# Optimization experiments

Hardware: AMD Instinct MI355X
Metric: run time of the kernel (lower is better)

The kernel has to match this reference:

```python
import jax, jax.numpy as jnp
import numpy as np

NUM_HEADS = 16
HEAD_DIM = 64
D_MODEL = NUM_HEADS * HEAD_DIM


def setup_inputs() -> dict:
    key = jax.random.key(0)
    ks = jax.random.split(key, 7)
    B, S = 2, 2048
    q = jax.random.normal(ks[0], (B, S, D_MODEL), dtype=jnp.float32)
    k = jax.random.normal(ks[1], (B, S, D_MODEL), dtype=jnp.float32)
    v = jax.random.normal(ks[2], (B, S, D_MODEL), dtype=jnp.float32)
    scale = 1.0 / np.sqrt(D_MODEL).astype(np.float32)
    w_q = jax.random.normal(ks[3], (D_MODEL, D_MODEL), dtype=jnp.float32) * scale
    w_k = jax.random.normal(ks[4], (D_MODEL, D_MODEL), dtype=jnp.float32) * scale
    w_v = jax.random.normal(ks[5], (D_MODEL, D_MODEL), dtype=jnp.float32) * scale
    w_o = jax.random.normal(ks[6], (D_MODEL, D_MODEL), dtype=jnp.float32) * scale
    return {"q": q, "k": k, "v": v, "w_q": w_q, "w_k": w_k, "w_v": w_v, "w_o": w_o}


def reference(q, k, v, w_q, w_k, w_v, w_o):
    B, S, _ = q.shape
    H, D = NUM_HEADS, HEAD_DIM
    # projections; q scaled by 1/sqrt(dim) as in the original (dim = per-head dim)
    qh = (q @ w_q) / jnp.sqrt(jnp.asarray(D, q.dtype))
    kh = k @ w_k
    vh = v @ w_v
    # tf.split(axis=-1) into H chunks == reshape [B,S,H,D]
    qh = qh.reshape(B, S, H, D)
    kh = kh.reshape(B, S, H, D)
    vh = vh.reshape(B, S, H, D)
    # keras Attention: scores = q @ k^T, softmax over keys, @ v (no extra scale)
    scores = jnp.einsum("bqhd,bkhd->bhqk", qh, kh)
    probs = jax.nn.softmax(scores, axis=-1)
    o = jnp.einsum("bhqk,bkhd->bqhd", probs, vh)
    o = o.reshape(B, S, H * D)
    return o @ w_o
```

## Files before the change

### kernel.cpp

```cpp
#include <hip/hip_runtime.h>
#include <hip/hip_bf16.h>


using bf16x8 = __attribute__((ext_vector_type(8))) short;
using f32x4  = __attribute__((ext_vector_type(4))) float;
using u32x4  = __attribute__((ext_vector_type(4))) unsigned;
typedef unsigned short u16;
using u16x4 = __attribute__((ext_vector_type(4))) u16;
using u16x8 = __attribute__((ext_vector_type(8))) u16;

#define GLDS16(g, l) __builtin_amdgcn_global_load_lds( \
    (const __attribute__((address_space(1))) void*)(g), \
    (__attribute__((address_space(3))) void*)(l), 16, 0, 0)

#if __has_builtin(__builtin_amdgcn_exp2f)
#define EXP2(x) __builtin_amdgcn_exp2f(x)
#else
#define EXP2(x) exp2f(x)
#endif

__device__ __forceinline__ void block_sync() {
  __builtin_amdgcn_sched_barrier(0);
  asm volatile("" ::: "memory");
  __builtin_amdgcn_s_barrier();
  asm volatile("" ::: "memory");
  __builtin_amdgcn_sched_barrier(0);
}

__device__ __forceinline__ u16 f2bf(float f) {
  unsigned u = __builtin_bit_cast(unsigned, f);
  u += 0x7fffu + ((u >> 16) & 1u);
  return (u16)(u >> 16);
}

__device__ __forceinline__ unsigned cvt_pk_bf16(float lo, float hi) {
  unsigned r;
  asm("v_cvt_pk_bf16_f32 %0, %1, %2" : "=v"(r) : "v"(lo), "v"(hi));
  return r;
}

__device__ __forceinline__ float fmax3(float a, float b, float c) {
  return fmaxf(fmaxf(a, b), c);
}

__global__ __launch_bounds__(256) void wtrans_kernel(
    const float* __restrict__ wq, const float* __restrict__ wk,
    const float* __restrict__ wv, const float* __restrict__ wo,
    u16* __restrict__ dst) {
  __shared__ float t[32][33];
  const int z = blockIdx.z;
  const float* src = (z == 0) ? wq : (z == 1) ? wk : (z == 2) ? wv : wo;
  u16* d = dst + (size_t)z * 1024 * 1024;
  const int tx = threadIdx.x & 31, ty = threadIdx.x >> 5;
  const int bx = blockIdx.x * 32, by = blockIdx.y * 32;
#pragma unroll
  for (int j = 0; j < 4; j++)
    t[ty + j * 8][tx] = src[(size_t)(by + ty + j * 8) * 1024 + bx + tx];
  __syncthreads();
#pragma unroll
  for (int j = 0; j < 4; j++)
    d[(size_t)(bx + ty + j * 8) * 1024 + by + tx] = f2bf(t[tx][ty + j * 8]);
}

__global__ __launch_bounds__(256, 3) void proj_kernel(
    const float* __restrict__ qf, const float* __restrict__ kf,
    const float* __restrict__ vf, const u16* __restrict__ WT,
    u16* __restrict__ Qh, u16* __restrict__ Kh, u16* __restrict__ Vt) {
  __shared__ u16 lds[24576];
  const int id = blockIdx.x;
  const int xcd = id & 7, l = id >> 3;
  const int z = l >> 5, rem = l & 31;
  const int by = xcd * 4 + (rem >> 3);
  const int bx = rem & 7;
  const int arow0 = by * 128, bcol0 = bx * 128;
  const float* A = (z == 0) ? qf : (z == 1) ? kf : vf;
  const u16* Bw = WT + (size_t)z * 1024 * 1024;

  const int tid = threadIdx.x;
  const int lane = tid & 63, wave = tid >> 6;
  const int lr = lane & 15, lg = lane >> 4;
  const int wr = (wave >> 1) * 64, wc = (wave & 1) * 64;
  const int ar = tid >> 3, ac = tid & 7;
  f32x4 acc[4][4] = {};

  f32x4 fa[4][2];
  u32x4 w[4];

  auto LOADA = [&](int kt) {
#pragma unroll
    for (int i = 0; i < 4; i++) {
      const float* ap = A + (size_t)(arow0 + i * 32 + ar) * 1024 + kt + ac * 8;
      fa[i][0] = *(const f32x4*)ap;
      fa[i][1] = *(const f32x4*)(ap + 4);
    }
  };
  auto GLDSB = [&](int kt, int nb) {
    u16* bd = lds + 8192 + nb * 8192;
#pragma unroll
    for (int i = 0; i < 4; i++) {
      int o = (i * 256 + tid) * 8;
      int row = o >> 6, ch = (o >> 3) & 7;
      int sc = (ch ^ (row & 7)) << 3;
      GLDS16(Bw + (size_t)(bcol0 + row) * 1024 + kt + sc, bd + o);
    }
  };
  auto CVT = [&]() {
#pragma unroll
    for (int i = 0; i < 4; i++) {
      u32x4 v = {cvt_pk_bf16(fa[i][0][0], fa[i][0][1]),
                 cvt_pk_bf16(fa[i][0][2], fa[i][0][3]),
                 cvt_pk_bf16(fa[i][1][0], fa[i][1][1]),
                 cvt_pk_bf16(fa[i][1][2], fa[i][1][3])};
      w[i] = v;
    }
  };
  auto WRITEA = [&]() {
#pragma unroll
    for (int i = 0; i < 4; i++) {
      int row = i * 32 + ar;
      *(u32x4*)&lds[row * 64 + ((ac ^ (row & 7)) << 3)] = w[i];
    }
  };
  auto MFMAK = [&](int cb) {
    const u16* Bb = lds + 8192 + cb * 8192;
#pragma unroll
    for (int kk = 0; kk < 2; kk++) {
      bf16x8 af[4], bfr[4];
      const int ke = kk * 32 + lg * 8;
#pragma unroll
      for (int m = 0; m < 4; m++) {
        int row = wr + m * 16 + lr;
        af[m] = *(const bf16x8*)&lds[row * 64 + (ke ^ ((row & 7) << 3))];
      }
#pragma unroll
      for (int n = 0; n < 4; n++) {
        int row = wc + n * 16 + lr;
        bfr[n] = *(const bf16x8*)&Bb[row * 64 + (ke ^ ((row & 7) << 3))];
      }
#pragma unroll
      for (int m = 0; m < 4; m++)
#pragma unroll
        for (int n = 0; n < 4; n++)
          acc[m][n] = __builtin_amdgcn_mfma_f32_16x16x32_bf16(af[m], bfr[n],
                                                              acc[m][n], 0, 0, 0);
    }
  };

#define PSTEP(KT, CB, MORE)                                                  \
  do {                                                                       \
    CVT();                                                                   \
    if (MORE) { LOADA((KT) + 64); GLDSB((KT) + 64, (CB) ^ 1); }              \
    WRITEA();                                                                \
    if (MORE)                                                                \
      asm volatile("s_waitcnt vmcnt(12) lgkmcnt(0)" ::: "memory");           \
    else                                                                     \
      asm volatile("s_waitcnt vmcnt(0) lgkmcnt(0)" ::: "memory");            \
    block_sync();                                                            \
    MFMAK(CB);                                                               \
    block_sync();                                                            \
  } while (0)

  LOADA(0);
  GLDSB(0, 0);
  for (int kt = 0; kt < 896; kt += 128) {
    PSTEP(kt, 0, true);
    PSTEP(kt + 64, 1, true);
  }
  PSTEP(896, 0, true);
  PSTEP(960, 1, false);
#undef PSTEP

  if (z == 2) {
    u16* T = lds;
    __syncthreads();
#pragma unroll
    for (int m = 0; m < 4; m++)
#pragma unroll
      for (int n = 0; n < 4; n++)
#pragma unroll
        for (int r = 0; r < 4; r++) {
          int sl = wr + m * 16 + lg * 4 + r;
          int cl = wc + n * 16 + lr;
          T[cl * 128 + (sl ^ ((cl & 7) << 3))] = f2bf(acc[m][n][r]);
        }
    __syncthreads();
    const int t = threadIdx.x;
    const int cl = t >> 1, s0 = (t & 1) * 64;
    const int gc = bcol0 + cl;
    const size_t vrow = ((size_t)(arow0 >> 11) * 16 + (gc >> 6)) * 64 + (gc & 63);
#pragma unroll
    for (int j = 0; j < 8; j++) {
      int sl = s0 + j * 8;
      u16x8 vv = *(const u16x8*)&T[cl * 128 + (sl ^ ((cl & 7) << 3))];
      *(u16x8*)&Vt[vrow * 2048 + (size_t)((arow0 & 2047) + sl)] = vv;
    }
  } else {
    const float scale = (z == 0) ? 0.18033688f : 1.0f;
    u16* dst = (z == 0) ? Qh : Kh;
#pragma unroll
    for (int m = 0; m < 4; m++)
#pragma unroll
      for (int n = 0; n < 4; n++)
#pragma unroll
        for (int r = 0; r < 4; r++) {
          int gr = arow0 + wr + m * 16 + lg * 4 + r;
          int gc = bcol0 + wc + n * 16 + lr;
          size_t idx = (((size_t)(gr >> 11) * 16 + (gc >> 6)) * 2048 +
                        (gr & 2047)) * 64 + (gc & 63);
          dst[idx] = f2bf(acc[m][n][r] * scale);
        }
  }
}

__global__ __launch_bounds__(512, 4) void attn_kernel(
    const u16* __restrict__ Qh, const u16* __restrict__ Kh,
    const u16* __restrict__ Vt, u16* __restrict__ Ob) {
  __shared__ u16 kt[4][64 * 64];
  __shared__ u16 vt[4][64 * 64];
  const int tid = threadIdx.x;
  const int lane = tid & 63, wave = tid >> 6;
  const int lr = lane & 15, lg = lane >> 4;
  const int id = blockIdx.x;
  const int swz = (id & 7) * 64 + (id >> 3);
  const int bh = swz >> 4;
  const int q0 = (swz & 15) * 128;
  const u16* Qb = Qh + ((size_t)bh * 2048 + q0) * 64;
  const u16* Kb = Kh + (size_t)bh * 2048 * 64;
  const u16* Vb = Vt + (size_t)bh * 64 * 2048;

  bf16x8 aq[2];
#pragma unroll
  for (int kk = 0; kk < 2; kk++)
    aq[kk] = *(const bf16x8*)(Qb + (wave * 16 + lr) * 64 + kk * 32 + lg * 8);

  const int hsw = (lr & 3) | (((lr >> 2) & 1) << 2);
  int koff[2][4];
#pragma unroll
  for (int n = 0; n < 4; n++) {
    int kr = 32 * (n >> 1) + 8 * (lr >> 2) + 4 * (n & 1) + (lr & 3);
#pragma unroll
    for (int kk = 0; kk < 2; kk++)
      koff[kk][n] = kr * 64 + ((kk * 32 + lg * 8) ^ (hsw << 3));
  }
  int voff[2][4];
#pragma unroll
  for (int n = 0; n < 4; n++) {
    int d = n * 16 + lr;
#pragma unroll
    for (int ks = 0; ks < 2; ks++)
      voff[ks][n] = d * 64 + ((ks * 32 + lg * 8) ^ ((d & 7) << 3));
  }

  const int o0 = tid * 8;
  const int srow = tid >> 3, sch = tid & 7;
  const int hk = (srow & 3) | (((srow >> 3) & 1) << 2);
  const u16* kg = Kb + (size_t)srow * 64 + ((sch ^ hk) << 3);
  const u16* vg = Vb + (size_t)srow * 2048 + ((sch ^ (srow & 7)) << 3);

  f32x4 oacc[4] = {};
  float mrun = -1e30f, lrun = 0.f;

  auto STAGE = [&](int t, int b) {
    GLDS16(kg + (size_t)t * 4096, &kt[0][0] + b * 4096 + o0);
    GLDS16(vg + t * 64, &vt[0][0] + b * 4096 + o0);
  };

  auto COMPUTE = [&](int cur) {
    f32x4 sacc[4] = {};
    __builtin_amdgcn_s_setprio(1);
#pragma unroll
    for (int kk = 0; kk < 2; kk++) {
#pragma unroll
      for (int n = 0; n < 4; n++) {
        bf16x8 ka = *(const bf16x8*)&kt[cur][koff[kk][n]];
        sacc[n] = __builtin_amdgcn_mfma_f32_16x16x32_bf16(ka, aq[kk],
                                                          sacc[n], 0, 0, 0);
      }
    }
    __builtin_amdgcn_s_setprio(0);
    float t0 = fmax3(sacc[0][0], sacc[0][1], sacc[0][2]);
    float t1 = fmax3(sacc[0][3], sacc[1][0], sacc[1][1]);
    float t2 = fmax3(sacc[1][2], sacc[1][3], sacc[2][0]);
    float t3 = fmax3(sacc[2][1], sacc[2][2], sacc[2][3]);
    float t4 = fmax3(sacc[3][0], sacc[3][1], sacc[3][2]);
    float mx = fmaxf(fmax3(t0, t1, t2), fmax3(t3, t4, sacc[3][3]));
    mx = fmaxf(mx, __shfl_xor(mx, 16));
    mx = fmaxf(mx, __shfl_xor(mx, 32));
    float mnew = fmaxf(mrun, mx);
    if (__all(mx - mrun <= 8.0f)) {
      mnew = mrun;
    } else {
      float corr = EXP2(mrun - mnew);
      mrun = mnew;
      lrun *= corr;
      float cr[4];
#pragma unroll
      for (int r = 0; r < 4; r++) cr[r] = __shfl(corr, lg * 4 + r);
#pragma unroll
      for (int n = 0; n < 4; n++)
#pragma unroll
        for (int r = 0; r < 4; r++) oacc[n][r] *= cr[r];
    }
    float psum = 0.f;
#pragma unroll
    for (int n = 0; n < 4; n++)
#pragma unroll
      for (int r = 0; r < 4; r++) {
        float p = EXP2(sacc[n][r] - mnew);
        sacc[n][r] = p;
        psum += p;
      }
    psum += __shfl_xor(psum, 16);
    psum += __shfl_xor(psum, 32);
    lrun += psum;
    u32x4 w0 = {cvt_pk_bf16(sacc[0][0], sacc[0][1]),
                cvt_pk_bf16(sacc[0][2], sacc[0][3]),
                cvt_pk_bf16(sacc[1][0], sacc[1][1]),
                cvt_pk_bf16(sacc[1][2], sacc[1][3])};
    u32x4 w1 = {cvt_pk_bf16(sacc[2][0], sacc[2][1]),
                cvt_pk_bf16(sacc[2][2], sacc[2][3]),
                cvt_pk_bf16(sacc[3][0], sacc[3][1]),
                cvt_pk_bf16(sacc[3][2], sacc[3][3])};
    bf16x8 pa0 = __builtin_bit_cast(bf16x8, w0);
    bf16x8 pa1 = __builtin_bit_cast(bf16x8, w1);
    __builtin_amdgcn_s_setprio(1);
#pragma unroll
    for (int ks = 0; ks < 2; ks++) {
      bf16x8 ap = ks ? pa1 : pa0;
      bf16x8 bv[4];
#pragma unroll
      for (int n = 0; n < 4; n++)
        bv[n] = *(const bf16x8*)&vt[cur][voff[ks][n]];
#pragma unroll
      for (int n = 0; n < 4; n++)
        oacc[n] = __builtin_amdgcn_mfma_f32_16x16x32_bf16(ap, bv[n],
                                                          oacc[n], 0, 0, 0);
    }
    __builtin_amdgcn_s_setprio(0);
  };

#define VMC6 asm volatile("s_waitcnt vmcnt(6)" ::: "memory")
#define VMC4 asm volatile("s_waitcnt vmcnt(4)" ::: "memory")
#define VMC2 asm volatile("s_waitcnt vmcnt(2)" ::: "memory")
#define VMC0 asm volatile("s_waitcnt vmcnt(0)" ::: "memory")
  STAGE(0, 0); STAGE(1, 1); STAGE(2, 2);
  for (int t = 0; t < 28; t += 4) {
    STAGE(t + 3, 3); VMC6; block_sync(); COMPUTE(0); block_sync();
    STAGE(t + 4, 0); VMC6; block_sync(); COMPUTE(1); block_sync();
    STAGE(t + 5, 1); VMC6; block_sync(); COMPUTE(2); block_sync();
    STAGE(t + 6, 2); VMC6; block_sync(); COMPUTE(3); block_sync();
  }
  STAGE(31, 3); VMC6; block_sync(); COMPUTE(0); block_sync();
  VMC4; block_sync(); COMPUTE(1); block_sync();
  VMC2; block_sync(); COMPUTE(2); block_sync();
  VMC0; block_sync(); COMPUTE(3);
#undef VMC6
#undef VMC4
#undef VMC2
#undef VMC0

  const int b = bh >> 4, h = bh & 15;
  float inv = 1.0f / lrun;
  float ivr[4];
#pragma unroll
  for (int r = 0; r < 4; r++) ivr[r] = __shfl(inv, lg * 4 + r);
#pragma unroll
  for (int r = 0; r < 4; r++) {
    int qrow = q0 + wave * 16 + lg * 4 + r;
#pragma unroll
    for (int n = 0; n < 4; n++) {
      int d = n * 16 + lr;
      Ob[((size_t)b * 2048 + qrow) * 1024 + h * 64 + d] = f2bf(oacc[n][r] * ivr[r]);
    }
  }
}

__global__ __launch_bounds__(256) void outproj_kernel(
    const u16* __restrict__ Ob, const u16* __restrict__ WoT,
    float* __restrict__ out) {
  __shared__ u16 ldsA[128 * 64];
  __shared__ u16 ldsB[64 * 64];
  const int tid = threadIdx.x;
  const int lane = tid & 63, wave = tid >> 6;
  const int lr = lane & 15, lg = lane >> 4;
  const int wr = (wave >> 1) * 64;
  const int wc = (wave & 1) * 32;
  const int id = blockIdx.x;
  const int xcd = id & 7, l = id >> 3;
  const int by = xcd * 4 + (l >> 4);
  const int bx = l & 15;
  const int arow0 = by * 128, bcol0 = bx * 64;
  f32x4 acc[4][2] = {};
  for (int kt = 0; kt < 1024; kt += 64) {
#pragma unroll
    for (int i = 0; i < 4; i++) {
      int o = (i * 256 + tid) * 8;
      int row = o >> 6, ch = (o >> 3) & 7;
      int sc = (ch ^ (row & 7)) << 3;
      GLDS16(Ob + (size_t)(arow0 + row) * 1024 + kt + sc, &ldsA[o]);
    }
#pragma unroll
    for (int i = 0; i < 2; i++) {
      int o = (i * 256 + tid) * 8;
      int row = o >> 6, ch = (o >> 3) & 7;
      int sc = (ch ^ (row & 7)) << 3;
      GLDS16(WoT + (size_t)(bcol0 + row) * 1024 + kt + sc, &ldsB[o]);
    }
    __syncthreads();
#pragma unroll
    for (int kk = 0; kk < 2; kk++) {
      const int ke = kk * 32 + lg * 8;
      bf16x8 af[4], bfr[2];
#pragma unroll
      for (int m = 0; m < 4; m++) {
        int row = wr + m * 16 + lr;
        af[m] = *(const bf16x8*)&ldsA[row * 64 + (ke ^ ((row & 7) << 3))];
      }
#pragma unroll
      for (int n = 0; n < 2; n++) {
        int row = wc + n * 16 + lr;
        bfr[n] = *(const bf16x8*)&ldsB[row * 64 + (ke ^ ((row & 7) << 3))];
      }
#pragma unroll
      for (int m = 0; m < 4; m++)
#pragma unroll
        for (int n = 0; n < 2; n++)
          acc[m][n] = __builtin_amdgcn_mfma_f32_16x16x32_bf16(af[m], bfr[n],
                                                              acc[m][n], 0, 0, 0);
    }
    __syncthreads();
  }
#pragma unroll
  for (int m = 0; m < 4; m++)
#pragma unroll
    for (int n = 0; n < 2; n++)
#pragma unroll
      for (int r = 0; r < 4; r++) {
        int gr = arow0 + wr + m * 16 + lg * 4 + r;
        int gc = bcol0 + wc + n * 16 + lr;
        out[(size_t)gr * 1024 + gc] = acc[m][n][r];
      }
}

extern "C" void kernel_launch(void* const* d_in, const int* in_sizes, int n_in,
                              void* d_out, int out_size, void* d_ws, size_t ws_size,
                              hipStream_t stream) {
  const float* q  = (const float*)d_in[0];
  const float* k  = (const float*)d_in[1];
  const float* v  = (const float*)d_in[2];
  const float* wq = (const float*)d_in[3];
  const float* wk = (const float*)d_in[4];
  const float* wv = (const float*)d_in[5];
  const float* wo = (const float*)d_in[6];
  float* out = (float*)d_out;
  char* ws = (char*)d_ws;

  u16* WT = (u16*)ws;
  u16* Qh = (u16*)(ws + (size_t)32 * 1024 * 1024);
  u16* Kh = (u16*)(ws + (size_t)40 * 1024 * 1024);
  u16* Vt = (u16*)(ws + (size_t)48 * 1024 * 1024);
  u16* Ob = (u16*)(ws + (size_t)56 * 1024 * 1024);

  wtrans_kernel<<<dim3(32, 32, 4), 256, 0, stream>>>(wq, wk, wv, wo, WT);
  proj_kernel<<<dim3(768), 256, 0, stream>>>(q, k, v, WT, Qh, Kh, Vt);
  attn_kernel<<<dim3(512), 512, 0, stream>>>(Qh, Kh, Vt, Ob);
  outproj_kernel<<<dim3(512), 256, 0, stream>>>(Ob, WT + (size_t)3 * 1024 * 1024, out);
}
```

Before: 121.6 us.

## Deepen fp32 A-tile prefetch to two stages and stage Q/K epilogue through LDS

The QKV projection kernel now double-buffers the fp32 A-operand registers, prefetching two k-steps ahead with adjusted vmcnt waits so global load latency overlaps more MFMA work. The Q/K epilogue also stops doing scattered 2-byte global stores. It writes the bf16 tile into swizzled LDS and then emits coalesced 16-byte row stores into the head-major layout. This costs more VGPRs for the second prefetch buffer and adds an extra LDS round trip and barriers in the epilogue.

```diff
diff --git a/kernel.cpp b/kernel.cpp
--- a/kernel.cpp
+++ b/kernel.cpp
@@ -83,15 +83,15 @@
   const int ar = tid >> 3, ac = tid & 7;
   f32x4 acc[4][4] = {};
 
-  f32x4 fa[4][2];
+  f32x4 fa[2][4][2];
   u32x4 w[4];
 
-  auto LOADA = [&](int kt) {
+  auto LOADA = [&](int kt, int p) {
 #pragma unroll
     for (int i = 0; i < 4; i++) {
       const float* ap = A + (size_t)(arow0 + i * 32 + ar) * 1024 + kt + ac * 8;
-      fa[i][0] = *(const f32x4*)ap;
-      fa[i][1] = *(const f32x4*)(ap + 4);
+      fa[p][i][0] = *(const f32x4*)ap;
+      fa[p][i][1] = *(const f32x4*)(ap + 4);
     }
   };
   auto GLDSB = [&](int kt, int nb) {
@@ -104,13 +104,13 @@
       GLDS16(Bw + (size_t)(bcol0 + row) * 1024 + kt + sc, bd + o);
     }
   };
-  auto CVT = [&]() {
+  auto CVT = [&](int p) {
 #pragma unroll
     for (int i = 0; i < 4; i++) {
-      u32x4 v = {cvt_pk_bf16(fa[i][0][0], fa[i][0][1]),
-                 cvt_pk_bf16(fa[i][0][2], fa[i][0][3]),
-                 cvt_pk_bf16(fa[i][1][0], fa[i][1][1]),
-                 cvt_pk_bf16(fa[i][1][2], fa[i][1][3])};
+      u32x4 v = {cvt_pk_bf16(fa[p][i][0][0], fa[p][i][0][1]),
+                 cvt_pk_bf16(fa[p][i][0][2], fa[p][i][0][3]),
+                 cvt_pk_bf16(fa[p][i][1][0], fa[p][i][1][1]),
+                 cvt_pk_bf16(fa[p][i][1][2], fa[p][i][1][3])};
       w[i] = v;
     }
   };
@@ -146,12 +146,19 @@
     }
   };
 
-#define PSTEP(KT, CB, MORE)                                                  \
+#define PSTEP(KT, CB, P, MODE)                                               \
   do {                                                                       \
-    CVT();                                                                   \
-    if (MORE) { LOADA((KT) + 64); GLDSB((KT) + 64, (CB) ^ 1); }              \
+    if (MODE == 2)                                                           \
+      asm volatile("s_waitcnt vmcnt(4)" ::: "memory");                       \
+    else                                                                     \
+      asm volatile("s_waitcnt vmcnt(12)" ::: "memory");                      \
+    CVT(P);                                                                  \
+    if (MODE <= 1) GLDSB((KT) + 64, (CB) ^ 1);                               \
+    if (MODE == 0) LOADA((KT) + 128, P);                                     \
     WRITEA();                                                                \
-    if (MORE)                                                                \
+    if (MODE == 0)                                                           \
+      asm volatile("s_waitcnt vmcnt(20) lgkmcnt(0)" ::: "memory");           \
+    else if (MODE == 1)                                                      \
       asm volatile("s_waitcnt vmcnt(12) lgkmcnt(0)" ::: "memory");           \
     else                                                                     \
       asm volatile("s_waitcnt vmcnt(0) lgkmcnt(0)" ::: "memory");            \
@@ -160,14 +167,15 @@
     block_sync();                                                            \
   } while (0)
 
-  LOADA(0);
+  LOADA(0, 0);
   GLDSB(0, 0);
+  LOADA(64, 1);
   for (int kt = 0; kt < 896; kt += 128) {
-    PSTEP(kt, 0, true);
-    PSTEP(kt + 64, 1, true);
-  }
-  PSTEP(896, 0, true);
-  PSTEP(960, 1, false);
+    PSTEP(kt, 0, 0, 0);
+    PSTEP(kt + 64, 1, 1, 0);
+  }
+  PSTEP(896, 0, 0, 1);
+  PSTEP(960, 1, 1, 2);
 #undef PSTEP
 
   if (z == 2) {
@@ -197,18 +205,30 @@
   } else {
     const float scale = (z == 0) ? 0.18033688f : 1.0f;
     u16* dst = (z == 0) ? Qh : Kh;
+    u16* T = lds;
+    __syncthreads();
 #pragma unroll
     for (int m = 0; m < 4; m++)
 #pragma unroll
       for (int n = 0; n < 4; n++)
 #pragma unroll
         for (int r = 0; r < 4; r++) {
-          int gr = arow0 + wr + m * 16 + lg * 4 + r;
-          int gc = bcol0 + wc + n * 16 + lr;
-          size_t idx = (((size_t)(gr >> 11) * 16 + (gc >> 6)) * 2048 +
-                        (gr & 2047)) * 64 + (gc & 63);
-          dst[idx] = f2bf(acc[m][n][r] * scale);
+          int sl = wr + m * 16 + lg * 4 + r;
+          int cl = wc + n * 16 + lr;
+          T[sl * 128 + (cl ^ ((sl & 7) << 3))] = f2bf(acc[m][n][r] * scale);
         }
+    __syncthreads();
+    const int t = threadIdx.x;
+    const int h2 = t >> 7, tt = t & 127;
+    const int rb = tt >> 3, c0 = (tt & 7) * 8;
+    const size_t bh = (size_t)(arow0 >> 11) * 16 + bx * 2 + h2;
+#pragma unroll
+    for (int j = 0; j < 8; j++) {
+      int row = j * 16 + rb;
+      int cl = h2 * 64 + c0;
+      u16x8 vv = *(const u16x8*)&T[row * 128 + (cl ^ ((row & 7) << 3))];
+      *(u16x8*)&dst[(bh * 2048 + (size_t)((arow0 & 2047) + row)) * 64 + c0] = vv;
+    }
   }
 }
 
```

New measurement: 161.3 us. +32.7%, slower.
